# Performance work log

Measured on AMD Instinct MI355X. Metric: run time of the kernel, lower is better.

Reference implementation:

```python
import jax, jax.numpy as jnp
import numpy as np

B, CIN, CCTX, K, V, T, KS = 8, 512, 512, 64, 256, 1024, 23
EPS = 1e-5


def _bn(z, gamma, beta):
    # train-mode BatchNorm1d over (batch, time) per channel, biased variance
    mean = jnp.mean(z, axis=(0, 2), keepdims=True)
    var = jnp.mean((z - mean) ** 2, axis=(0, 2), keepdims=True)
    return (z - mean) * jax.lax.rsqrt(var + EPS) * gamma[None, :, None] + beta[None, :, None]


def setup_inputs() -> dict:
    key = jax.random.key(0)
    ks = jax.random.split(key, 10)
    x = jax.random.normal(ks[0], (B, CIN, T), dtype=jnp.float32)
    context = jax.random.normal(ks[1], (B, CCTX, T), dtype=jnp.float32)
    Wq = jax.random.normal(ks[2], (K, CIN), dtype=jnp.float32) * (CIN ** -0.5)
    bq = jnp.zeros((K,), dtype=jnp.float32)
    Wk = jax.random.normal(ks[3], (K, CCTX), dtype=jnp.float32) * (CCTX ** -0.5)
    bk = jnp.zeros((K,), dtype=jnp.float32)
    Wv = jax.random.normal(ks[4], (V, CCTX), dtype=jnp.float32) * (CCTX ** -0.5)
    bv = jnp.zeros((V,), dtype=jnp.float32)
    gamma_q = jnp.ones((K,), dtype=jnp.float32)
    beta_q = jnp.zeros((K,), dtype=jnp.float32)
    gamma_v = jnp.ones((V,), dtype=jnp.float32)
    beta_v = jnp.zeros((V,), dtype=jnp.float32)
    pos_w = jax.random.normal(ks[5], (K, KS), dtype=jnp.float32) * (KS ** -0.5)
    pos_b = jnp.zeros((K,), dtype=jnp.float32)
    return {"x": x, "context": context, "Wq": Wq, "bq": bq, "Wk": Wk, "bk": bk,
            "Wv": Wv, "bv": bv, "gamma_q": gamma_q, "beta_q": beta_q,
            "gamma_v": gamma_v, "beta_v": beta_v, "pos_w": pos_w, "pos_b": pos_b}


def reference(x, context, Wq, bq, Wk, bk, Wv, bv,
              gamma_q, beta_q, gamma_v, beta_v, pos_w, pos_b):
    # 1x1 conv1d == channel matmul
    queries = jnp.einsum('bct,kc->bkt', x, Wq) + bq[None, :, None]          # (B,K,T)
    keys = jnp.einsum('bct,kc->bkt', context, Wk) + bk[None, :, None]       # (B,K,T)
    values = jnp.einsum('bct,vc->bvt', context, Wv) + bv[None, :, None]     # (B,V,T)

    norm_keys = jax.nn.softmax(keys, axis=-1)                               # softmax over T
    queries = _bn(queries, gamma_q, beta_q)
    values = _bn(values, gamma_v, beta_v)

    q_t = jnp.transpose(queries, (0, 2, 1))                                 # (B,T,K)
    v_t = jnp.transpose(values, (0, 2, 1))                                  # (B,T,V)

    content_lambda = jnp.einsum('bkt,btv->bkv', norm_keys, v_t)             # (B,K,V)

    # positional conv2d: kernel (K,1,KS,1), padding (KS//2, 0) along T
    lhs = v_t[:, None, :, :]                                                # (B,1,T,V)
    rhs = pos_w[:, None, :, None]                                           # (K,1,KS,1)
    pl = jax.lax.conv_general_dilated(
        lhs, rhs, window_strides=(1, 1),
        padding=[(KS // 2, KS // 2), (0, 0)],
        dimension_numbers=('NCHW', 'OIHW', 'NCHW'))
    pl = pl + pos_b[None, :, None, None]                                    # (B,K,T,V)
    pl = jnp.transpose(pl, (0, 2, 1, 3))                                    # (B,T,K,V)

    content_out = jnp.einsum('btk,bkv->btv', q_t, content_lambda)           # (B,T,V)
    positional_out = jnp.einsum('btk,btkv->btv', q_t, pl)                   # (B,T,V)

    return jnp.transpose(content_out + positional_out, (0, 2, 1))           # (B,V,T)
```

## Files before the change

kernel.cpp:

```cpp
#include <hip/hip_runtime.h>
#include <math.h>

#define B_ 8
#define CIN_ 512
#define K_ 64
#define V_ 256
#define T_ 1024
#define KS_ 23
#define EPS_ 1e-5f
#define NTC_ 16

typedef __attribute__((ext_vector_type(8))) short bf16x8;
typedef __attribute__((ext_vector_type(4))) float f32x4;

__device__ __forceinline__ unsigned short f2bf(float f) {
    union { float f; unsigned u; } x; x.f = f;
    unsigned r = x.u + 0x7fffu + ((x.u >> 16) & 1u);
    return (unsigned short)(r >> 16);
}
__device__ __forceinline__ float bf2f(unsigned short h) {
    union { unsigned u; float f; } x; x.u = ((unsigned)h) << 16;
    return x.f;
}

__global__ __launch_bounds__(256) void prep_kernel(
    const float* __restrict__ x, const float* __restrict__ ctx,
    const float* __restrict__ Wq, const float* __restrict__ Wk,
    const float* __restrict__ Wv,
    unsigned short* __restrict__ xT, unsigned short* __restrict__ cT,
    unsigned short* __restrict__ Wb, float* __restrict__ stat)
{
    __shared__ unsigned short sh[64][72];
    const int tid = threadIdx.x;
    const int id = blockIdx.x;
    if (id < 2048) {
        const int t0 = (id & 15) * 64, c0 = ((id >> 4) & 7) * 64;
        const int z = id >> 7, b = z & 7, which = z >> 3;
        const float* src = which ? ctx : x;
        unsigned short* dst = which ? cT : xT;
        const int cl = tid >> 2, qq = tid & 3;
        const float* row = src + ((size_t)b * CIN_ + c0 + cl) * T_ + t0 + qq * 16;
        #pragma unroll
        for (int u = 0; u < 4; u++) {
            float4 f = *(const float4*)(row + 4 * u);
            sh[qq * 16 + 4 * u + 0][cl] = f2bf(f.x);
            sh[qq * 16 + 4 * u + 1][cl] = f2bf(f.y);
            sh[qq * 16 + 4 * u + 2][cl] = f2bf(f.z);
            sh[qq * 16 + 4 * u + 3][cl] = f2bf(f.w);
        }
        __syncthreads();
        const int tl = tid >> 2;
        unsigned short* orow = dst + ((size_t)b * T_ + t0 + tl) * CIN_ + c0 + qq * 16;
        *(bf16x8*)(orow)     = *(bf16x8*)&sh[tl][qq * 16];
        *(bf16x8*)(orow + 8) = *(bf16x8*)&sh[tl][qq * 16 + 8];
    } else {
        const int wid = id - 2048;
        if (wid == 0 && tid < 160)
            ((float4*)stat)[tid] = make_float4(0.f, 0.f, 0.f, 0.f);
        const int i4 = wid * 256 + tid;
        const int n1 = K_ * CIN_ / 4, n2 = 2 * K_ * CIN_ / 4;
        const float* src; int off;
        if (i4 < n1)      { src = Wq; off = i4; }
        else if (i4 < n2) { src = Wk; off = i4 - n1; }
        else              { src = Wv; off = i4 - n2; }
        float4 f = ((const float4*)src)[off];
        ushort4 h;
        h.x = f2bf(f.x); h.y = f2bf(f.y); h.z = f2bf(f.z); h.w = f2bf(f.w);
        *(ushort4*)(Wb + (size_t)i4 * 4) = h;
    }
}

__global__ __launch_bounds__(256) void proj_mfma4(
    const unsigned short* __restrict__ xT, const unsigned short* __restrict__ cT,
    const unsigned short* __restrict__ Wb,
    const float* __restrict__ bq, const float* __restrict__ bk,
    const float* __restrict__ bv,
    float* __restrict__ k_buf, float* __restrict__ v_raw,
    unsigned short* __restrict__ qT, float* __restrict__ stat,
    float* __restrict__ kml)
{
    __shared__ unsigned short Wt[64][72];
    __shared__ unsigned short Xt[128][72];
    const int tid = threadIdx.x;
    const int b = blockIdx.z, t0 = blockIdx.x * 128, yb = blockIdx.y;

    const unsigned short* in; const unsigned short* W; const float* bias;
    float* outp = nullptr; int ch0 = 0; float* ssum = nullptr; float* ssq = nullptr;
    if (yb == 0)      { in = xT; W = Wb;             bias = bq;
                        ssum = stat; ssq = stat + 64; ch0 = 0; }
    else if (yb == 1) { in = cT; W = Wb + K_ * CIN_; bias = bk;
                        outp = k_buf + (size_t)b * K_ * T_; }
    else { int m0 = (yb - 2) * 64; in = cT;
           W = Wb + 2 * K_ * CIN_ + (size_t)m0 * CIN_; bias = bv + m0;
           outp = v_raw + ((size_t)b * V_ + m0) * T_;
           ssum = stat + 128; ssq = stat + 384; ch0 = m0; }

    const int lane = tid & 63, w = tid >> 6;
    const int col = lane & 15, quad = lane >> 4;
    const int wm = tid >> 2, wp = tid & 3;
    const int xt = tid >> 1, xh = tid & 1;

    f32x4 acc[8];
    #pragma unroll
    for (int j = 0; j < 8; j++) acc[j] = (f32x4){0.f, 0.f, 0.f, 0.f};

    for (int c0 = 0; c0 < CIN_; c0 += 64) {
        {
            const unsigned short* ws = W + (size_t)wm * CIN_ + c0 + wp * 16;
            *(bf16x8*)&Wt[wm][wp * 16]     = *(const bf16x8*)(ws);
            *(bf16x8*)&Wt[wm][wp * 16 + 8] = *(const bf16x8*)(ws + 8);
            const unsigned short* xs = in + ((size_t)b * T_ + t0 + xt) * CIN_ + c0 + xh * 32;
            #pragma unroll
            for (int u = 0; u < 4; u++)
                *(bf16x8*)&Xt[xt][xh * 32 + 8 * u] = *(const bf16x8*)(xs + 8 * u);
        }
        __syncthreads();
        #pragma unroll
        for (int ks = 0; ks < 2; ks++) {
            const int kc = ks * 32 + quad * 8;
            bf16x8 af = *(bf16x8*)&Wt[w * 16 + col][kc];
            #pragma unroll
            for (int j = 0; j < 8; j++) {
                bf16x8 bfr = *(bf16x8*)&Xt[j * 16 + col][kc];
                acc[j] = __builtin_amdgcn_mfma_f32_16x16x32_bf16(af, bfr, acc[j], 0, 0, 0);
            }
        }
        __syncthreads();
    }

    float bias_v[4], s[4], sq[4], mr[4], lr[4];
    #pragma unroll
    for (int r = 0; r < 4; r++) {
        bias_v[r] = bias[w * 16 + quad * 4 + r];
        s[r] = 0.f; sq[r] = 0.f; mr[r] = -1e30f; lr[r] = 0.f;
    }
    #pragma unroll
    for (int j = 0; j < 8; j++) {
        float o[4];
        #pragma unroll
        for (int r = 0; r < 4; r++) {
            o[r] = acc[j][r] + bias_v[r];
            s[r] += o[r]; sq[r] += o[r] * o[r];
        }
        if (yb == 0) {
            ushort4 h;
            h.x = f2bf(o[0]); h.y = f2bf(o[1]); h.z = f2bf(o[2]); h.w = f2bf(o[3]);
            *(ushort4*)(qT + ((size_t)b * T_ + t0 + j * 16 + col) * K_ + w * 16 + quad * 4) = h;
        } else {
            #pragma unroll
            for (int r = 0; r < 4; r++)
                outp[(size_t)(w * 16 + quad * 4 + r) * T_ + t0 + j * 16 + col] = o[r];
            if (yb == 1) {
                #pragma unroll
                for (int r = 0; r < 4; r++) {
                    float mn = fmaxf(mr[r], o[r]);
                    lr[r] = lr[r] * __expf(mr[r] - mn) + __expf(o[r] - mn);
                    mr[r] = mn;
                }
            }
        }
    }
    if (yb == 1) {
        #pragma unroll
        for (int r = 0; r < 4; r++) {
            float m = mr[r], l = lr[r];
            #pragma unroll
            for (int off = 1; off < 16; off <<= 1) {
                float mo = __shfl_xor(m, off, 64);
                float lo = __shfl_xor(l, off, 64);
                float mn = fmaxf(m, mo);
                l = l * __expf(m - mn) + lo * __expf(mo - mn);
                m = mn;
            }
            if (col == 0) {
                int row = w * 16 + quad * 4 + r;
                float* p = kml + (((size_t)b * K_ + row) * 8 + (t0 >> 7)) * 2;
                p[0] = m; p[1] = l;
            }
        }
    } else {
        #pragma unroll
        for (int r = 0; r < 4; r++) {
            float sv = s[r], qv = sq[r];
            #pragma unroll
            for (int off = 1; off < 16; off <<= 1) {
                sv += __shfl_xor(sv, off, 64);
                qv += __shfl_xor(qv, off, 64);
            }
            if (col == 0) {
                int ch = ch0 + w * 16 + quad * 4 + r;
                atomicAdd(&ssum[ch], sv);
                atomicAdd(&ssq[ch], qv);
            }
        }
    }
}

__global__ __launch_bounds__(256) void lambda_kernel4(
    const float* __restrict__ k_buf, const float* __restrict__ v_raw,
    const float* __restrict__ kml, float* __restrict__ clp)
{
    __shared__ __align__(16) float nks[K_][68];
    __shared__ __align__(16) float vls[64][68];
    __shared__ float mrow[64], lrow[64];
    const int tid = threadIdx.x;
    const int b = blockIdx.z, v0 = blockIdx.y * 64, tc = blockIdx.x, t0 = tc * 64;

    if (tid < 64) {
        const float2* p = (const float2*)(kml + ((size_t)b * K_ + tid) * 16);
        float m = -1e30f, l = 0.f;
        #pragma unroll
        for (int sgi = 0; sgi < 8; sgi++) {
            float2 ml = p[sgi];
            float mn = fmaxf(m, ml.x);
            l = l * __expf(m - mn) + ml.y * __expf(ml.x - mn);
            m = mn;
        }
        mrow[tid] = m; lrow[tid] = 1.f / l;
    }
    __syncthreads();
    {
        const int r = tid >> 2, q = tid & 3;
        const float* nrow = k_buf + ((size_t)b * K_ + r) * T_ + t0;
        const float* vrow = v_raw + ((size_t)b * V_ + v0 + r) * T_ + t0;
        const float mr = mrow[r], li = lrow[r];
        #pragma unroll
        for (int i = 0; i < 4; i++) {
            int c4 = q + 4 * i;
            float4 g = *(const float4*)(nrow + 4 * c4);
            g.x = __expf(g.x - mr) * li; g.y = __expf(g.y - mr) * li;
            g.z = __expf(g.z - mr) * li; g.w = __expf(g.w - mr) * li;
            *(float4*)&nks[r][4 * c4] = g;
            float4 h = *(const float4*)(vrow + 4 * c4);
            vls[4 * c4 + 0][r] = h.x; vls[4 * c4 + 1][r] = h.y;
            vls[4 * c4 + 2][r] = h.z; vls[4 * c4 + 3][r] = h.w;
        }
    }
    __syncthreads();
    const int tv = tid & 15, tk = tid >> 4;
    float4 acc[4];
    #pragma unroll
    for (int i = 0; i < 4; i++) acc[i] = make_float4(0.f, 0.f, 0.f, 0.f);
    for (int tt = 0; tt < 16; tt++) {
        float4 w0 = *(float4*)&vls[4 * tt + 0][4 * tv];
        float4 w1 = *(float4*)&vls[4 * tt + 1][4 * tv];
        float4 w2 = *(float4*)&vls[4 * tt + 2][4 * tv];
        float4 w3 = *(float4*)&vls[4 * tt + 3][4 * tv];
        #pragma unroll
        for (int i = 0; i < 4; i++) {
            float4 n = *(float4*)&nks[4 * tk + i][4 * tt];
            acc[i] += w0 * n.x + w1 * n.y + w2 * n.z + w3 * n.w;
        }
    }
    #pragma unroll
    for (int i = 0; i < 4; i++)
        *(float4*)&clp[(((size_t)b * NTC_ + tc) * K_ + 4 * tk + i) * V_ + v0 + 4 * tv] = acc[i];
}

__global__ __launch_bounds__(256) void prep_cl_kernel2(
    const float* __restrict__ clp, const float* __restrict__ stat,
    const float* __restrict__ gq, const float* __restrict__ betaq,
    const float* __restrict__ gv, const float* __restrict__ betav,
    unsigned short* __restrict__ clb2, float* __restrict__ hterm)
{
    __shared__ float qsc[64], qsh[64], red[4][64];
    const int tid = threadIdx.x;
    const int b = blockIdx.y, v0 = blockIdx.x * 64;
    const float inv_n = 1.f / (B_ * T_);
    if (tid < 64) {
        float mean = stat[tid] * inv_n;
        float var  = stat[64 + tid] * inv_n - mean * mean;
        float sc = gq[tid] * rsqrtf(var + EPS_);
        qsc[tid] = sc; qsh[tid] = betaq[tid] - mean * sc;
    }
    const int vl = tid & 63, kq = tid >> 6;
    const int c = v0 + vl;
    float vmean = stat[128 + c] * inv_n;
    float vvar  = stat[384 + c] * inv_n - vmean * vmean;
    float vsv = gv[c] * rsqrtf(vvar + EPS_);
    float vhv = betav[c] - vmean * vsv;
    __syncthreads();
    float h = 0.f;
    for (int kk = 0; kk < 16; kk++) {
        int k = kq * 16 + kk;
        float a = 0.f;
        #pragma unroll
        for (int tc = 0; tc < NTC_; tc++)
            a += clp[(((size_t)b * NTC_ + tc) * K_ + k) * V_ + c];
        float clbv = a * vsv + vhv;
        h += qsh[k] * clbv;
        clb2[((size_t)b * V_ + c) * K_ + k] = f2bf(clbv * qsc[k]);
    }
    red[kq][vl] = h;
    __syncthreads();
    if (tid < 64)
        hterm[(size_t)b * V_ + v0 + tid] =
            red[0][tid] + red[1][tid] + red[2][tid] + red[3][tid];
}

__global__ __launch_bounds__(256) void out_kernel4(
    const unsigned short* __restrict__ qT, const unsigned short* __restrict__ clb2,
    const float* __restrict__ hterm, const float* __restrict__ v_raw,
    const float* __restrict__ stat,
    const float* __restrict__ gq, const float* __restrict__ betaq,
    const float* __restrict__ gv, const float* __restrict__ betav,
    const float* __restrict__ pos_w, const float* __restrict__ pos_b,
    float* __restrict__ out)
{
    __shared__ unsigned short qTt[64][72];
    __shared__ unsigned short clv[64][72];
    __shared__ float vs2T[88][68];
    __shared__ float qpt[64][24];
    __shared__ float pws[64][24];
    __shared__ float qsc[64], qsh[64];
    __shared__ float consts[24];
    __shared__ float hvs[64];
    const int tid = threadIdx.x;
    const int b = blockIdx.z, v0 = blockIdx.y * 64, t0 = blockIdx.x * 64;
    const float inv_n = 1.f / (B_ * T_);

    if (tid < 64) {
        float mean = stat[tid] * inv_n;
        float var  = stat[64 + tid] * inv_n - mean * mean;
        float sc = gq[tid] * rsqrtf(var + EPS_);
        qsc[tid] = sc; qsh[tid] = betaq[tid] - mean * sc;
        hvs[tid] = hterm[(size_t)b * V_ + v0 + tid];
    }
    {
        const int rl = tid >> 2, part = tid & 3;
        const unsigned short* qs = qT + ((size_t)b * T_ + t0 + rl) * K_ + part * 16;
        *(bf16x8*)&qTt[rl][part * 16]     = *(const bf16x8*)(qs);
        *(bf16x8*)&qTt[rl][part * 16 + 8] = *(const bf16x8*)(qs + 8);
        const unsigned short* cs = clb2 + ((size_t)b * V_ + v0 + rl) * K_ + part * 16;
        *(bf16x8*)&clv[rl][part * 16]     = *(const bf16x8*)(cs);
        *(bf16x8*)&clv[rl][part * 16 + 8] = *(const bf16x8*)(cs + 8);
    }
    {
        const int vl = tid >> 2, qq = tid & 3;
        const int c = v0 + vl;
        float vmean = stat[128 + c] * inv_n;
        float vvar  = stat[384 + c] * inv_n - vmean * vmean;
        float vsv = gv[c] * rsqrtf(vvar + EPS_);
        float vhv = betav[c] - vmean * vsv;
        const float* vrow = v_raw + ((size_t)b * V_ + c) * T_;
        #pragma unroll
        for (int i = 0; i < 22; i++) {
            int cc = qq + 4 * i;
            if (cc < 86) {
                int t = t0 + cc - 11;
                vs2T[cc][vl] = (t >= 0 && t < T_) ? vrow[t] * vsv + vhv : 0.f;
            }
        }
    }
    __syncthreads();

    for (int idx = tid; idx < K_ * 24; idx += 256) {
        int k = idx / 24, s = idx % 24;
        pws[k][s] = qsc[k] * (s < KS_ ? pos_w[k * KS_ + s] : pos_b[k]);
    }
    if (tid < 24) {
        float cs = 0.f;
        for (int k = 0; k < K_; k++)
            cs += qsh[k] * (tid < KS_ ? pos_w[k * KS_ + tid] : pos_b[k]);
        consts[tid] = cs;
    }
    __syncthreads();

    {
        const int t = tid >> 2, sg = tid & 3, s0 = sg * 6;
        float a[6];
        #pragma unroll
        for (int u = 0; u < 6; u++) a[u] = consts[s0 + u];
        #pragma unroll
        for (int kb = 0; kb < 8; kb++) {
            bf16x8 qv = *(bf16x8*)&qTt[t][kb * 8];
            #pragma unroll
            for (int j = 0; j < 8; j++) {
                float q = bf2f((unsigned short)qv[j]);
                #pragma unroll
                for (int u = 0; u < 6; u++) a[u] += q * pws[kb * 8 + j][s0 + u];
            }
        }
        #pragma unroll
        for (int u = 0; u < 6; u++) qpt[t][s0 + u] = a[u];
    }
    __syncthreads();

    const int lane = tid & 63, w = tid >> 6;
    const int col = lane & 15, quad = lane >> 4;

    f32x4 acc[4];
    #pragma unroll
    for (int tf = 0; tf < 4; tf++) acc[tf] = (f32x4){0.f, 0.f, 0.f, 0.f};

    #pragma unroll
    for (int ks = 0; ks < 2; ks++) {
        const int kc = ks * 32 + quad * 8;
        bf16x8 af = *(bf16x8*)&clv[w * 16 + col][kc];
        #pragma unroll
        for (int tf = 0; tf < 4; tf++) {
            bf16x8 bq = *(bf16x8*)&qTt[tf * 16 + col][kc];
            acc[tf] = __builtin_amdgcn_mfma_f32_16x16x32_bf16(af, bq, acc[tf], 0, 0, 0);
        }
    }

    const int vb = w * 16 + quad * 4;
    float4 hv4 = *(float4*)&hvs[vb];
    #pragma unroll
    for (int tf = 0; tf < 4; tf++) {
        const int lt = tf * 16 + col;
        float qv[24];
        #pragma unroll
        for (int u = 0; u < 6; u++)
            *(float4*)&qv[4 * u] = *(float4*)&qpt[lt][4 * u];
        float4 a; a.x = acc[tf][0]; a.y = acc[tf][1]; a.z = acc[tf][2]; a.w = acc[tf][3];
        #pragma unroll
        for (int s = 0; s < KS_; s++) {
            float4 wv = *(float4*)&vs2T[lt + s][vb];
            a.x += qv[s] * wv.x; a.y += qv[s] * wv.y;
            a.z += qv[s] * wv.z; a.w += qv[s] * wv.w;
        }
        float base = qv[23];
        a.x += base + hv4.x; a.y += base + hv4.y;
        a.z += base + hv4.z; a.w += base + hv4.w;
        float* ap = (float*)&a;
        #pragma unroll
        for (int r = 0; r < 4; r++)
            out[((size_t)b * V_ + v0 + vb + r) * T_ + t0 + lt] = ap[r];
    }
}

extern "C" void kernel_launch(void* const* d_in, const int* in_sizes, int n_in,
                              void* d_out, int out_size, void* d_ws, size_t ws_size,
                              hipStream_t stream)
{
    const float* x     = (const float*)d_in[0];
    const float* ctx   = (const float*)d_in[1];
    const float* Wq    = (const float*)d_in[2];
    const float* bq    = (const float*)d_in[3];
    const float* Wk    = (const float*)d_in[4];
    const float* bk    = (const float*)d_in[5];
    const float* Wv    = (const float*)d_in[6];
    const float* bv    = (const float*)d_in[7];
    const float* gq    = (const float*)d_in[8];
    const float* betaq = (const float*)d_in[9];
    const float* gv    = (const float*)d_in[10];
    const float* betav = (const float*)d_in[11];
    const float* pos_w = (const float*)d_in[12];
    const float* pos_b = (const float*)d_in[13];
    float* out = (float*)d_out;

    float* ws    = (float*)d_ws;
    float* k_buf = ws;
    float* v_raw = k_buf + (size_t)B_ * K_ * T_;
    float* clp   = v_raw + (size_t)B_ * V_ * T_;
    float* stat  = clp + (size_t)B_ * NTC_ * K_ * V_;
    float* hterm = stat + 640;
    float* kml   = hterm + (size_t)B_ * V_;
    unsigned short* xT   = (unsigned short*)(kml + (size_t)B_ * K_ * 16);
    unsigned short* cT   = xT + (size_t)B_ * T_ * CIN_;
    unsigned short* Wb   = cT + (size_t)B_ * T_ * CIN_;
    unsigned short* qT   = Wb + (size_t)(2 * K_ + V_) * CIN_;
    unsigned short* clb2 = qT + (size_t)B_ * T_ * K_;

    prep_kernel<<<dim3(2048 + 192), 256, 0, stream>>>(
        x, ctx, Wq, Wk, Wv, xT, cT, Wb, stat);
    proj_mfma4<<<dim3(T_ / 128, 6, B_), 256, 0, stream>>>(
        xT, cT, Wb, bq, bk, bv, k_buf, v_raw, qT, stat, kml);
    lambda_kernel4<<<dim3(NTC_, V_ / 64, B_), 256, 0, stream>>>(k_buf, v_raw, kml, clp);
    prep_cl_kernel2<<<dim3(V_ / 64, B_), 256, 0, stream>>>(
        clp, stat, gq, betaq, gv, betav, clb2, hterm);
    out_kernel4<<<dim3(T_ / 64, V_ / 64, B_), 256, 0, stream>>>(
        qT, clb2, hterm, v_raw, stat, gq, betaq, gv, betav, pos_w, pos_b, out);
}
```

Before: 158.4 us.

## Use direct global-to-LDS loads with swizzle, halve lambda partials, split prep_cl

Measured after the change: 150.3 us. 5.1% less time.

```diff
diff --git a/kernel.cpp b/kernel.cpp
--- a/kernel.cpp
+++ b/kernel.cpp
@@ -8,7 +8,7 @@
 #define T_ 1024
 #define KS_ 23
 #define EPS_ 1e-5f
-#define NTC_ 16
+#define NTC_ 8
 
 typedef __attribute__((ext_vector_type(8))) short bf16x8;
 typedef __attribute__((ext_vector_type(4))) float f32x4;
@@ -21,6 +21,12 @@
 __device__ __forceinline__ float bf2f(unsigned short h) {
     union { unsigned u; float f; } x; x.u = ((unsigned)h) << 16;
     return x.f;
+}
+
+__device__ __forceinline__ void gload16(const unsigned short* g, unsigned short* l) {
+    __builtin_amdgcn_global_load_lds(
+        (const __attribute__((address_space(1))) unsigned int*)(const void*)g,
+        (__attribute__((address_space(3))) unsigned int*)(void*)l, 16, 0, 0);
 }
 
 __global__ __launch_bounds__(256) void prep_kernel(
@@ -55,8 +61,13 @@
         *(bf16x8*)(orow + 8) = *(bf16x8*)&sh[tl][qq * 16 + 8];
     } else {
         const int wid = id - 2048;
-        if (wid == 0 && tid < 160)
-            ((float4*)stat)[tid] = make_float4(0.f, 0.f, 0.f, 0.f);
+        if (wid == 0) {
+            #pragma unroll
+            for (int i = 0; i < 3; i++) {
+                int idx = tid + i * 256;
+                if (idx < 672) ((float4*)stat)[idx] = make_float4(0.f, 0.f, 0.f, 0.f);
+            }
+        }
         const int i4 = wid * 256 + tid;
         const int n1 = K_ * CIN_ / 4, n2 = 2 * K_ * CIN_ / 4;
         const float* src; int off;
@@ -70,7 +81,7 @@
     }
 }
 
-__global__ __launch_bounds__(256) void proj_mfma4(
+__global__ __launch_bounds__(256) void proj_mfma5(
     const unsigned short* __restrict__ xT, const unsigned short* __restrict__ cT,
     const unsigned short* __restrict__ Wb,
     const float* __restrict__ bq, const float* __restrict__ bk,
@@ -79,8 +90,10 @@
     unsigned short* __restrict__ qT, float* __restrict__ stat,
     float* __restrict__ kml)
 {
-    __shared__ unsigned short Wt[64][72];
-    __shared__ unsigned short Xt[128][72];
+    __shared__ __align__(16) unsigned short SM[64 * 64 + 128 * 64];
+    unsigned short* Wt = SM;
+    unsigned short* Xt = SM + 64 * 64;
+
     const int tid = threadIdx.x;
     const int b = blockIdx.z, t0 = blockIdx.x * 128, yb = blockIdx.y;
 
@@ -97,31 +110,47 @@
 
     const int lane = tid & 63, w = tid >> 6;
     const int col = lane & 15, quad = lane >> 4;
-    const int wm = tid >> 2, wp = tid & 3;
-    const int xt = tid >> 1, xh = tid & 1;
+
+    const int gW0 = (0 * 4 + w) * 64 + lane, rW0 = gW0 >> 3;
+    const int gW1 = (1 * 4 + w) * 64 + lane, rW1 = gW1 >> 3;
+    const unsigned short* sW0 = W + (size_t)rW0 * CIN_ + (((gW0 & 7) ^ (rW0 & 7)) * 8);
+    const unsigned short* sW1 = W + (size_t)rW1 * CIN_ + (((gW1 & 7) ^ (rW1 & 7)) * 8);
+    unsigned short* dW0 = Wt + (0 * 4 + w) * 512;
+    unsigned short* dW1 = Wt + (1 * 4 + w) * 512;
+
+    const int gX0 = (0 * 4 + w) * 64 + lane, rX0 = gX0 >> 3;
+    const int gX1 = (1 * 4 + w) * 64 + lane, rX1 = gX1 >> 3;
+    const int gX2 = (2 * 4 + w) * 64 + lane, rX2 = gX2 >> 3;
+    const int gX3 = (3 * 4 + w) * 64 + lane, rX3 = gX3 >> 3;
+    const size_t xbase = (size_t)b * T_ + t0;
+    const unsigned short* sX0 = in + (xbase + rX0) * CIN_ + (((gX0 & 7) ^ (rX0 & 7)) * 8);
+    const unsigned short* sX1 = in + (xbase + rX1) * CIN_ + (((gX1 & 7) ^ (rX1 & 7)) * 8);
+    const unsigned short* sX2 = in + (xbase + rX2) * CIN_ + (((gX2 & 7) ^ (rX2 & 7)) * 8);
+    const unsigned short* sX3 = in + (xbase + rX3) * CIN_ + (((gX3 & 7) ^ (rX3 & 7)) * 8);
+    unsigned short* dX0 = Xt + (0 * 4 + w) * 512;
+    unsigned short* dX1 = Xt + (1 * 4 + w) * 512;
+    unsigned short* dX2 = Xt + (2 * 4 + w) * 512;
+    unsigned short* dX3 = Xt + (3 * 4 + w) * 512;
 
     f32x4 acc[8];
     #pragma unroll
     for (int j = 0; j < 8; j++) acc[j] = (f32x4){0.f, 0.f, 0.f, 0.f};
 
     for (int c0 = 0; c0 < CIN_; c0 += 64) {
-        {
-            const unsigned short* ws = W + (size_t)wm * CIN_ + c0 + wp * 16;
-            *(bf16x8*)&Wt[wm][wp * 16]     = *(const bf16x8*)(ws);
-            *(bf16x8*)&Wt[wm][wp * 16 + 8] = *(const bf16x8*)(ws + 8);
-            const unsigned short* xs = in + ((size_t)b * T_ + t0 + xt) * CIN_ + c0 + xh * 32;
-            #pragma unroll
-            for (int u = 0; u < 4; u++)
-                *(bf16x8*)&Xt[xt][xh * 32 + 8 * u] = *(const bf16x8*)(xs + 8 * u);
-        }
+        gload16(sW0 + c0, dW0);
+        gload16(sW1 + c0, dW1);
+        gload16(sX0 + c0, dX0);
+        gload16(sX1 + c0, dX1);
+        gload16(sX2 + c0, dX2);
+        gload16(sX3 + c0, dX3);
         __syncthreads();
         #pragma unroll
         for (int ks = 0; ks < 2; ks++) {
-            const int kc = ks * 32 + quad * 8;
-            bf16x8 af = *(bf16x8*)&Wt[w * 16 + col][kc];
+            const int kc = ((ks * 4 + quad) ^ (col & 7)) * 8;
+            bf16x8 af = *(bf16x8*)&Wt[(w * 16 + col) * 64 + kc];
             #pragma unroll
             for (int j = 0; j < 8; j++) {
-                bf16x8 bfr = *(bf16x8*)&Xt[j * 16 + col][kc];
+                bf16x8 bfr = *(bf16x8*)&Xt[(j * 16 + col) * 64 + kc];
                 acc[j] = __builtin_amdgcn_mfma_f32_16x16x32_bf16(af, bfr, acc[j], 0, 0, 0);
             }
         }
@@ -145,7 +174,7 @@
         if (yb == 0) {
             ushort4 h;
             h.x = f2bf(o[0]); h.y = f2bf(o[1]); h.z = f2bf(o[2]); h.w = f2bf(o[3]);
-            *(ushort4*)(qT + ((size_t)b * T_ + t0 + j * 16 + col) * K_ + w * 16 + quad * 4) = h;
+            *(ushort4*)&SM[(j * 16 + col) * 72 + w * 16 + quad * 4] = h;
         } else {
             #pragma unroll
             for (int r = 0; r < 4; r++)
@@ -160,6 +189,14 @@
             }
         }
     }
+    if (yb == 0) {
+        __syncthreads();
+        const int tr = tid >> 1, h2 = tid & 1;
+        unsigned short* dq = qT + ((size_t)b * T_ + t0 + tr) * K_ + h2 * 32;
+        #pragma unroll
+        for (int u = 0; u < 4; u++)
+            *(bf16x8*)(dq + u * 8) = *(bf16x8*)&SM[tr * 72 + h2 * 32 + u * 8];
+    }
     if (yb == 1) {
         #pragma unroll
         for (int r = 0; r < 4; r++) {
@@ -196,7 +233,7 @@
     }
 }
 
-__global__ __launch_bounds__(256) void lambda_kernel4(
+__global__ __launch_bounds__(256) void lambda_kernel5(
     const float* __restrict__ k_buf, const float* __restrict__ v_raw,
     const float* __restrict__ kml, float* __restrict__ clp)
 {
@@ -204,7 +241,7 @@
     __shared__ __align__(16) float vls[64][68];
     __shared__ float mrow[64], lrow[64];
     const int tid = threadIdx.x;
-    const int b = blockIdx.z, v0 = blockIdx.y * 64, tc = blockIdx.x, t0 = tc * 64;
+    const int b = blockIdx.z, v0 = blockIdx.y * 64, tc = blockIdx.x;
 
     if (tid < 64) {
         const float2* p = (const float2*)(kml + ((size_t)b * K_ + tid) * 16);
@@ -219,37 +256,43 @@
         mrow[tid] = m; lrow[tid] = 1.f / l;
     }
     __syncthreads();
-    {
-        const int r = tid >> 2, q = tid & 3;
-        const float* nrow = k_buf + ((size_t)b * K_ + r) * T_ + t0;
-        const float* vrow = v_raw + ((size_t)b * V_ + v0 + r) * T_ + t0;
-        const float mr = mrow[r], li = lrow[r];
-        #pragma unroll
-        for (int i = 0; i < 4; i++) {
-            int c4 = q + 4 * i;
-            float4 g = *(const float4*)(nrow + 4 * c4);
-            g.x = __expf(g.x - mr) * li; g.y = __expf(g.y - mr) * li;
-            g.z = __expf(g.z - mr) * li; g.w = __expf(g.w - mr) * li;
-            *(float4*)&nks[r][4 * c4] = g;
-            float4 h = *(const float4*)(vrow + 4 * c4);
-            vls[4 * c4 + 0][r] = h.x; vls[4 * c4 + 1][r] = h.y;
-            vls[4 * c4 + 2][r] = h.z; vls[4 * c4 + 3][r] = h.w;
-        }
-    }
-    __syncthreads();
+
+    const int r = tid >> 2, q = tid & 3;
     const int tv = tid & 15, tk = tid >> 4;
     float4 acc[4];
     #pragma unroll
     for (int i = 0; i < 4; i++) acc[i] = make_float4(0.f, 0.f, 0.f, 0.f);
-    for (int tt = 0; tt < 16; tt++) {
-        float4 w0 = *(float4*)&vls[4 * tt + 0][4 * tv];
-        float4 w1 = *(float4*)&vls[4 * tt + 1][4 * tv];
-        float4 w2 = *(float4*)&vls[4 * tt + 2][4 * tv];
-        float4 w3 = *(float4*)&vls[4 * tt + 3][4 * tv];
-        #pragma unroll
-        for (int i = 0; i < 4; i++) {
-            float4 n = *(float4*)&nks[4 * tk + i][4 * tt];
-            acc[i] += w0 * n.x + w1 * n.y + w2 * n.z + w3 * n.w;
+
+    for (int c2 = 0; c2 < 2; c2++) {
+        const int t0 = (tc * 2 + c2) * 64;
+        if (c2) __syncthreads();
+        {
+            const float* nrow = k_buf + ((size_t)b * K_ + r) * T_ + t0;
+            const float* vrow = v_raw + ((size_t)b * V_ + v0 + r) * T_ + t0;
+            const float mr = mrow[r], li = lrow[r];
+            #pragma unroll
+            for (int i = 0; i < 4; i++) {
+                int c4 = q + 4 * i;
+                float4 g = *(const float4*)(nrow + 4 * c4);
+                g.x = __expf(g.x - mr) * li; g.y = __expf(g.y - mr) * li;
+                g.z = __expf(g.z - mr) * li; g.w = __expf(g.w - mr) * li;
+                *(float4*)&nks[r][4 * c4] = g;
+                float4 h = *(const float4*)(vrow + 4 * c4);
+                vls[4 * c4 + 0][r] = h.x; vls[4 * c4 + 1][r] = h.y;
+                vls[4 * c4 + 2][r] = h.z; vls[4 * c4 + 3][r] = h.w;
+            }
+        }
+        __syncthreads();
+        for (int tt = 0; tt < 16; tt++) {
+            float4 w0 = *(float4*)&vls[4 * tt + 0][4 * tv];
+            float4 w1 = *(float4*)&vls[4 * tt + 1][4 * tv];
+            float4 w2 = *(float4*)&vls[4 * tt + 2][4 * tv];
+            float4 w3 = *(float4*)&vls[4 * tt + 3][4 * tv];
+            #pragma unroll
+            for (int i = 0; i < 4; i++) {
+                float4 n = *(float4*)&nks[4 * tk + i][4 * tt];
+                acc[i] += w0 * n.x + w1 * n.y + w2 * n.z + w3 * n.w;
+            }
         }
     }
     #pragma unroll
@@ -257,7 +300,7 @@
         *(float4*)&clp[(((size_t)b * NTC_ + tc) * K_ + 4 * tk + i) * V_ + v0 + 4 * tv] = acc[i];
 }
 
-__global__ __launch_bounds__(256) void prep_cl_kernel2(
+__global__ __launch_bounds__(256) void prep_cl_kernel3(
     const float* __restrict__ clp, const float* __restrict__ stat,
     const float* __restrict__ gq, const float* __restrict__ betaq,
     const float* __restrict__ gv, const float* __restrict__ betav,
@@ -265,7 +308,7 @@
 {
     __shared__ float qsc[64], qsh[64], red[4][64];
     const int tid = threadIdx.x;
-    const int b = blockIdx.y, v0 = blockIdx.x * 64;
+    const int b = blockIdx.y, v0 = blockIdx.x * 64, kz = blockIdx.z;
     const float inv_n = 1.f / (B_ * T_);
     if (tid < 64) {
         float mean = stat[tid] * inv_n;
@@ -281,8 +324,9 @@
     float vhv = betav[c] - vmean * vsv;
     __syncthreads();
     float h = 0.f;
-    for (int kk = 0; kk < 16; kk++) {
-        int k = kq * 16 + kk;
+    #pragma unroll
+    for (int kk = 0; kk < 4; kk++) {
+        int k = kz * 16 + kq * 4 + kk;
         float a = 0.f;
         #pragma unroll
         for (int tc = 0; tc < NTC_; tc++)
@@ -294,8 +338,8 @@
     red[kq][vl] = h;
     __syncthreads();
     if (tid < 64)
-        hterm[(size_t)b * V_ + v0 + tid] =
-            red[0][tid] + red[1][tid] + red[2][tid] + red[3][tid];
+        atomicAdd(&hterm[(size_t)b * V_ + v0 + tid],
+                  red[0][tid] + red[1][tid] + red[2][tid] + red[3][tid]);
 }
 
 __global__ __launch_bounds__(256) void out_kernel4(
@@ -465,10 +509,10 @@
 
     prep_kernel<<<dim3(2048 + 192), 256, 0, stream>>>(
         x, ctx, Wq, Wk, Wv, xT, cT, Wb, stat);
-    proj_mfma4<<<dim3(T_ / 128, 6, B_), 256, 0, stream>>>(
+    proj_mfma5<<<dim3(T_ / 128, 6, B_), 256, 0, stream>>>(
         xT, cT, Wb, bq, bk, bv, k_buf, v_raw, qT, stat, kml);
-    lambda_kernel4<<<dim3(NTC_, V_ / 64, B_), 256, 0, stream>>>(k_buf, v_raw, kml, clp);
-    prep_cl_kernel2<<<dim3(V_ / 64, B_), 256, 0, stream>>>(
+    lambda_kernel5<<<dim3(NTC_, V_ / 64, B_), 256, 0, stream>>>(k_buf, v_raw, kml, clp);
+    prep_cl_kernel3<<<dim3(V_ / 64, B_, 4), 256, 0, stream>>>(
         clp, stat, gq, betaq, gv, betav, clb2, hterm);
     out_kernel4<<<dim3(T_ / 64, V_ / 64, B_), 256, 0, stream>>>(
         qT, clb2, hterm, v_raw, stat, gq, betaq, gv, betav, pos_w, pos_b, out);
```
